# Kernel tuning notes

Measured on AMD Instinct MI355X. Metric: run time of the kernel, lower is better.

## Reference

```python
import jax, jax.numpy as jnp
import numpy as np
from jax import lax

FPLANE = 256
RATIO = 0.5
C_SHIFT = int(FPLANE * RATIO)  # 128
HALF = C_SHIFT // 2            # 64


def setup_inputs() -> dict:
    key = jax.random.key(0)
    k_x, k_wl, k_bl, k_wr, k_br = jax.random.split(key, 5)
    T, C, H, W = 64, FPLANE, 56, 56
    x = jax.random.normal(k_x, (T, C, H, W), dtype=jnp.float32)
    # Conv3d(HALF -> 1, kernel (3,3,3)); original inits to zero, we use small
    # random weights so the gated path is non-trivial for kernel testing.
    scale = 1.0 / np.sqrt(HALF * 27)
    w_l = jax.random.normal(k_wl, (1, HALF, 3, 3, 3), dtype=jnp.float32) * scale
    b_l = jax.random.normal(k_bl, (1,), dtype=jnp.float32) * 0.01
    w_r = jax.random.normal(k_wr, (1, HALF, 3, 3, 3), dtype=jnp.float32) * scale
    b_r = jax.random.normal(k_br, (1,), dtype=jnp.float32) * 0.01
    return {"x": x, "w_l": w_l, "b_l": b_l, "w_r": w_r, "b_r": b_r}


def _cyclic_pad_t(x):
    # x: (1, C, T, H, W) -> pad 1 frame cyclically along T
    return jnp.concatenate([x[:, :, -1:], x, x[:, :, :1]], axis=2)


def _conv3d(x, w, b):
    # temporal padding VALID (input is cyclically pre-padded), spatial SAME
    y = lax.conv_general_dilated(
        x, w, window_strides=(1, 1, 1),
        padding=[(0, 0), (1, 1), (1, 1)],
        dimension_numbers=("NCDHW", "OIDHW", "NCDHW"))
    return y + b[None, :, None, None, None]


def reference(x, w_l, b_l, w_r, b_r):
    # x: (T, C, H, W) -> (1, C, T, H, W)
    x5 = x.transpose(1, 0, 2, 3)[None]
    x_l = x5[:, :HALF]                 # (1, half, T, H, W)
    x_r = x5[:, HALF:C_SHIFT]
    x_keep = x5[:, C_SHIFT:]

    gate_l = jnp.tanh(_conv3d(_cyclic_pad_t(x_l), w_l, b_l))  # (1,1,T,H,W)
    gate_r = jnp.tanh(_conv3d(_cyclic_pad_t(x_r), w_r, b_r))

    y_l = gate_l * x_l
    y_r = gate_r * x_r
    y_l = jnp.roll(y_l, -1, axis=2) + (x_l - y_l)
    y_r = jnp.roll(y_r, 1, axis=2) + (x_r - y_r)

    y_all = jnp.concatenate([y_l, y_r, x_keep], axis=1)  # (1, C, T, H, W)
    return y_all[0].transpose(1, 0, 2, 3)                # (T, C, H, W)
```

## Files before the change

### kernel.cpp

```cpp
#include <hip/hip_runtime.h>
#include <math.h>

#define T_DIM 64
#define C_DIM 256
#define H_DIM 56
#define W_DIM 56
#define HW    (H_DIM * W_DIM)
#define HW4   (HW / 4)
#define CHW   (C_DIM * HW)
#define THW   (T_DIM * HW)

typedef float nt_float4 __attribute__((ext_vector_type(4)));

__device__ __forceinline__ float rfl(float v) {
    return __int_as_float(__builtin_amdgcn_readfirstlane(__float_as_int(v)));
}

template<int S>
__global__ __launch_bounds__(256) void gate_copy_kernel(
    const float* __restrict__ x,
    const float* __restrict__ w_l,
    const float* __restrict__ w_r,
    float* __restrict__ pbuf,
    float* __restrict__ out)
{
    constexpr int CPG   = 64 / S;
    constexpr int NGATE = 2 * S * 32;

    const int p = blockIdx.x;

    if (p >= NGATE) {
        const int qq     = p - NGATE;
        const int tchunk = qq / 392;
        const int bx2    = qq - tchunk * 392;
        const int tid    = 128 * HW4 + bx2 * 256 + (int)threadIdx.x;
        const int t0     = tchunk * 16;

        const nt_float4* xn4 = (const nt_float4*)x;
        nt_float4*       on4 = (nt_float4*)out;
        const size_t ts = C_DIM * HW4;

        #pragma unroll 4
        for (int i = 0; i < 16; ++i) {
            const size_t idx = (size_t)(t0 + i) * ts + tid;
            nt_float4 v = __builtin_nontemporal_load(&xn4[idx]);
            __builtin_nontemporal_store(v, &on4[idx]);
        }
        return;
    }

    const int xcd = p & 7;
    const int s   = p >> 3;
    const int sg  = xcd * (2 * S / 8) + (s >> 5);
    const int tq  = s & 31;
    const int side = sg / S;
    const int g    = sg & (S - 1);

    const int waveid = __builtin_amdgcn_readfirstlane((int)(threadIdx.x >> 6));
    const int hh = waveid & 1;
    const int t  = tq * 2 + (waveid >> 1);

    const int lane = threadIdx.x & 63;
    const int wg   = lane & 15;
    const int rg   = lane >> 4;
    const bool act = (wg < 14);
    const int w0   = act ? wg * 4 : 52;
    const int r0   = hh * 28 + rg * 7;
    const bool have_l = (wg > 0);
    const bool have_r = (wg < 13);

    const float* wtab = (side ? w_r : w_l) + g * CPG * 27;
    const int c0 = side * 64 + g * CPG;

    const int tm = (t + 63) & 63, tp = (t + 1) & 63;
    const float* tbase[3] = { x + (size_t)tm * CHW,
                              x + (size_t)t  * CHW,
                              x + (size_t)tp * CHW };

    float acc[7][4];
    #pragma unroll
    for (int j = 0; j < 7; ++j)
        #pragma unroll
        for (int k = 0; k < 4; ++k) acc[j][k] = 0.f;

    #pragma unroll 1
    for (int ci = 0; ci < CPG; ++ci) {
        float wgt[27];
        #pragma unroll
        for (int k = 0; k < 27; ++k) wgt[k] = rfl(wtab[ci * 27 + k]);

        #pragma unroll
        for (int dt = 0; dt < 3; ++dt) {
            const float* plane = tbase[dt] + (size_t)(c0 + ci) * HW;

            #pragma unroll
            for (int s9 = 0; s9 < 9; ++s9) {
                const int sr = r0 - 1 + s9;
                bool rv = true;
                int  srow = sr;
                if (s9 == 0)      { rv = (sr >= 0);     srow = rv ? sr : 0; }
                else if (s9 == 8) { rv = (sr < H_DIM);  srow = rv ? sr : (H_DIM - 1); }

                const float* row = plane + srow * W_DIM;
                float4 m  = *(const float4*)(row + w0);
                float  fl = __shfl_up(m.w, 1);
                float  fr = __shfl_down(m.x, 1);

                float f0 = have_l ? fl : 0.f;
                float f1 = m.x, f2 = m.y, f3 = m.z, f4v = m.w;
                float f5 = have_r ? fr : 0.f;
                if ((s9 == 0 || s9 == 8) && !rv) {
                    f0 = 0.f; f1 = 0.f; f2 = 0.f; f3 = 0.f; f4v = 0.f; f5 = 0.f;
                }
                float f[6] = { f0, f1, f2, f3, f4v, f5 };

                const int jlo = (s9 >= 2) ? s9 - 2 : 0;
                const int jhi = (s9 <= 6) ? s9 : 6;
                #pragma unroll
                for (int j = jlo; j <= jhi; ++j) {
                    const int dh = s9 - j;
                    const float w0t = wgt[dt * 9 + dh * 3 + 0];
                    const float w1t = wgt[dt * 9 + dh * 3 + 1];
                    const float w2t = wgt[dt * 9 + dh * 3 + 2];
                    #pragma unroll
                    for (int k = 0; k < 4; ++k)
                        acc[j][k] += w0t * f[k] + w1t * f[k + 1] + w2t * f[k + 2];
                }
            }
        }
    }

    if (act) {
        float* pp = pbuf + (size_t)sg * THW
                         + (size_t)t * HW + r0 * W_DIM + w0;
        #pragma unroll
        for (int j = 0; j < 7; ++j) {
            float4 v; v.x = acc[j][0]; v.y = acc[j][1]; v.z = acc[j][2]; v.w = acc[j][3];
            *(float4*)(pp + j * W_DIM) = v;
        }
    }
}

template<int S>
__global__ __launch_bounds__(256) void reduce_tanh_kernel(
    const float* __restrict__ pbuf,
    float* __restrict__ gbuf,
    const float* __restrict__ b_l,
    const float* __restrict__ b_r)
{
    const int i = blockIdx.x * 256 + threadIdx.x;
    const float4* p4 = (const float4*)pbuf;
    float4* g4 = (float4*)gbuf;

    float4 a = {0.f,0.f,0.f,0.f}, b = {0.f,0.f,0.f,0.f};
    #pragma unroll
    for (int g = 0; g < S; ++g) {
        float4 va = p4[(size_t)g       * (THW/4) + i];
        float4 vb = p4[(size_t)(S + g) * (THW/4) + i];
        a.x += va.x; a.y += va.y; a.z += va.z; a.w += va.w;
        b.x += vb.x; b.y += vb.y; b.z += vb.z; b.w += vb.w;
    }
    const float bl = b_l[0], br = b_r[0];
    float4 gl, gr;
    gl.x = tanhf(a.x + bl); gl.y = tanhf(a.y + bl);
    gl.z = tanhf(a.z + bl); gl.w = tanhf(a.w + bl);
    gr.x = tanhf(b.x + br); gr.y = tanhf(b.y + br);
    gr.z = tanhf(b.z + br); gr.w = tanhf(b.w + br);
    g4[i]           = gl;
    g4[(THW/4) + i] = gr;
}

__global__ __launch_bounds__(256) void combine_kernel(
    const float* __restrict__ x,
    const float* __restrict__ g,
    float* __restrict__ out)
{
    const int tid = blockIdx.x * 256 + threadIdx.x;
    const int t0  = blockIdx.y * 16;
    const int c   = tid / HW4;
    const int gb  = tid - c * HW4;

    const float4* x4 = (const float4*)x;
    nt_float4*    on4 = (nt_float4*)out;
    const size_t  ts = C_DIM * HW4;
    const size_t  base = tid;

    if (c < 64) {
        const float4* gl4 = (const float4*)g;
        float4 xv = x4[(size_t)t0 * ts + base];
        float4 g0 = gl4[t0 * HW4 + gb];
        #pragma unroll 4
        for (int i = 0; i < 16; ++i) {
            const int t  = t0 + i;
            const int tp = (t + 1) & 63;
            float4 xn = x4[(size_t)tp * ts + base];
            float4 g1 = gl4[tp * HW4 + gb];
            nt_float4 r;
            r.x = xv.x - g0.x * xv.x + g1.x * xn.x;
            r.y = xv.y - g0.y * xv.y + g1.y * xn.y;
            r.z = xv.z - g0.z * xv.z + g1.z * xn.z;
            r.w = xv.w - g0.w * xv.w + g1.w * xn.w;
            __builtin_nontemporal_store(r, &on4[(size_t)t * ts + base]);
            xv = xn; g0 = g1;
        }
    } else {
        const float4* gr4 = (const float4*)(g + THW);
        const int tmi = (t0 + 63) & 63;
        float4 xm = x4[(size_t)tmi * ts + base];
        float4 gm = gr4[tmi * HW4 + gb];
        #pragma unroll 4
        for (int i = 0; i < 16; ++i) {
            const int t = t0 + i;
            float4 xv = x4[(size_t)t * ts + base];
            float4 g0 = gr4[t * HW4 + gb];
            nt_float4 r;
            r.x = xv.x - g0.x * xv.x + gm.x * xm.x;
            r.y = xv.y - g0.y * xv.y + gm.y * xm.y;
            r.z = xv.z - g0.z * xv.z + gm.z * xm.z;
            r.w = xv.w - g0.w * xv.w + gm.w * xm.w;
            __builtin_nontemporal_store(r, &on4[(size_t)t * ts + base]);
            xm = xv; gm = g0;
        }
    }
}

template<int S>
static void launch_all(const float* x, const float* w_l, const float* b_l,
                       const float* w_r, const float* b_r,
                       float* out, float* ws, hipStream_t stream)
{
    float* pbuf = ws;
    float* gbuf = ws + (size_t)(2 * S) * THW;

    const int ngate = 2 * S * 32;
    const int ncopy = 392 * 4;
    gate_copy_kernel<S><<<ngate + ncopy, 256, 0, stream>>>(x, w_l, w_r, pbuf, out);
    reduce_tanh_kernel<S><<<THW / 4 / 256, 256, 0, stream>>>(pbuf, gbuf, b_l, b_r);
    combine_kernel<<<dim3(392, 4), 256, 0, stream>>>(x, gbuf, out);
}

extern "C" void kernel_launch(void* const* d_in, const int* in_sizes, int n_in,
                              void* d_out, int out_size, void* d_ws, size_t ws_size,
                              hipStream_t stream) {
    const float* x   = (const float*)d_in[0];
    const float* w_l = (const float*)d_in[1];
    const float* b_l = (const float*)d_in[2];
    const float* w_r = (const float*)d_in[3];
    const float* b_r = (const float*)d_in[4];
    float* out = (float*)d_out;
    float* ws  = (float*)d_ws;

    const size_t plane_bytes = (size_t)THW * 4;
    if (ws_size >= 34 * plane_bytes)
        launch_all<16>(x, w_l, b_l, w_r, b_r, out, ws, stream);
    else if (ws_size >= 18 * plane_bytes)
        launch_all<8>(x, w_l, b_l, w_r, b_r, out, ws, stream);
    else
        launch_all<4>(x, w_l, b_l, w_r, b_r, out, ws, stream);
}
```

Measured before the change: 110.2 us.

## Fuse channel-partial reduction and tanh into gate kernel via LDS

The gate conv kernel now assigns 16 input channels to each of four waves in a block and reduces the four partial sums through shared memory, then applies the bias and tanh directly. This replaces writing many per-group partial planes to the workspace and running a separate reduce/tanh kernel. It removes a large global-memory round trip and a kernel launch. The cost is fewer gate blocks, each with a longer serial channel loop, plus a block barrier.

```diff
diff --git a/kernel.cpp b/kernel.cpp
--- a/kernel.cpp
+++ b/kernel.cpp
@@ -16,17 +16,16 @@
     return __int_as_float(__builtin_amdgcn_readfirstlane(__float_as_int(v)));
 }
 
-template<int S>
 __global__ __launch_bounds__(256) void gate_copy_kernel(
     const float* __restrict__ x,
     const float* __restrict__ w_l,
+    const float* __restrict__ b_l,
     const float* __restrict__ w_r,
-    float* __restrict__ pbuf,
+    const float* __restrict__ b_r,
+    float* __restrict__ gbuf,
     float* __restrict__ out)
 {
-    constexpr int CPG   = 64 / S;
-    constexpr int NGATE = 2 * S * 32;
-
+    constexpr int NGATE = 256;
     const int p = blockIdx.x;
 
     if (p >= NGATE) {
@@ -49,17 +48,16 @@
         return;
     }
 
-    const int xcd = p & 7;
-    const int s   = p >> 3;
-    const int sg  = xcd * (2 * S / 8) + (s >> 5);
-    const int tq  = s & 31;
-    const int side = sg / S;
-    const int g    = sg & (S - 1);
+    __shared__ float4 red[4][7][64];
+
+    const int xcd  = p & 7;
+    const int r    = p >> 3;
+    const int tl   = r & 7;
+    const int side = (r >> 3) & 1;
+    const int hh   = (r >> 4) & 1;
+    const int t    = xcd * 8 + tl;
 
     const int waveid = __builtin_amdgcn_readfirstlane((int)(threadIdx.x >> 6));
-    const int hh = waveid & 1;
-    const int t  = tq * 2 + (waveid >> 1);
-
     const int lane = threadIdx.x & 63;
     const int wg   = lane & 15;
     const int rg   = lane >> 4;
@@ -69,8 +67,8 @@
     const bool have_l = (wg > 0);
     const bool have_r = (wg < 13);
 
-    const float* wtab = (side ? w_r : w_l) + g * CPG * 27;
-    const int c0 = side * 64 + g * CPG;
+    const float* wtab = (side ? w_r : w_l) + waveid * 16 * 27;
+    const int c0 = side * 64 + waveid * 16;
 
     const int tm = (t + 63) & 63, tp = (t + 1) & 63;
     const float* tbase[3] = { x + (size_t)tm * CHW,
@@ -84,7 +82,7 @@
         for (int k = 0; k < 4; ++k) acc[j][k] = 0.f;
 
     #pragma unroll 1
-    for (int ci = 0; ci < CPG; ++ci) {
+    for (int ci = 0; ci < 16; ++ci) {
         float wgt[27];
         #pragma unroll
         for (int k = 0; k < 27; ++k) wgt[k] = rfl(wtab[ci * 27 + k]);
@@ -130,44 +128,29 @@
         }
     }
 
-    if (act) {
-        float* pp = pbuf + (size_t)sg * THW
+    #pragma unroll
+    for (int j = 0; j < 7; ++j) {
+        float4 v; v.x = acc[j][0]; v.y = acc[j][1]; v.z = acc[j][2]; v.w = acc[j][3];
+        red[waveid][j][lane] = v;
+    }
+    __syncthreads();
+
+    if (waveid == 0 && act) {
+        const float bias = side ? b_r[0] : b_l[0];
+        float* pp = gbuf + (size_t)side * THW
                          + (size_t)t * HW + r0 * W_DIM + w0;
         #pragma unroll
         for (int j = 0; j < 7; ++j) {
-            float4 v; v.x = acc[j][0]; v.y = acc[j][1]; v.z = acc[j][2]; v.w = acc[j][3];
+            float4 a = red[0][j][lane], b2 = red[1][j][lane];
+            float4 c = red[2][j][lane], d  = red[3][j][lane];
+            float4 v;
+            v.x = tanhf((a.x + b2.x) + (c.x + d.x) + bias);
+            v.y = tanhf((a.y + b2.y) + (c.y + d.y) + bias);
+            v.z = tanhf((a.z + b2.z) + (c.z + d.z) + bias);
+            v.w = tanhf((a.w + b2.w) + (c.w + d.w) + bias);
             *(float4*)(pp + j * W_DIM) = v;
         }
     }
-}
-
-template<int S>
-__global__ __launch_bounds__(256) void reduce_tanh_kernel(
-    const float* __restrict__ pbuf,
-    float* __restrict__ gbuf,
-    const float* __restrict__ b_l,
-    const float* __restrict__ b_r)
-{
-    const int i = blockIdx.x * 256 + threadIdx.x;
-    const float4* p4 = (const float4*)pbuf;
-    float4* g4 = (float4*)gbuf;
-
-    float4 a = {0.f,0.f,0.f,0.f}, b = {0.f,0.f,0.f,0.f};
-    #pragma unroll
-    for (int g = 0; g < S; ++g) {
-        float4 va = p4[(size_t)g       * (THW/4) + i];
-        float4 vb = p4[(size_t)(S + g) * (THW/4) + i];
-        a.x += va.x; a.y += va.y; a.z += va.z; a.w += va.w;
-        b.x += vb.x; b.y += vb.y; b.z += vb.z; b.w += vb.w;
-    }
-    const float bl = b_l[0], br = b_r[0];
-    float4 gl, gr;
-    gl.x = tanhf(a.x + bl); gl.y = tanhf(a.y + bl);
-    gl.z = tanhf(a.z + bl); gl.w = tanhf(a.w + bl);
-    gr.x = tanhf(b.x + br); gr.y = tanhf(b.y + br);
-    gr.z = tanhf(b.z + br); gr.w = tanhf(b.w + br);
-    g4[i]           = gl;
-    g4[(THW/4) + i] = gr;
 }
 
 __global__ __launch_bounds__(256) void combine_kernel(
@@ -224,21 +207,6 @@
     }
 }
 
-template<int S>
-static void launch_all(const float* x, const float* w_l, const float* b_l,
-                       const float* w_r, const float* b_r,
-                       float* out, float* ws, hipStream_t stream)
-{
-    float* pbuf = ws;
-    float* gbuf = ws + (size_t)(2 * S) * THW;
-
-    const int ngate = 2 * S * 32;
-    const int ncopy = 392 * 4;
-    gate_copy_kernel<S><<<ngate + ncopy, 256, 0, stream>>>(x, w_l, w_r, pbuf, out);
-    reduce_tanh_kernel<S><<<THW / 4 / 256, 256, 0, stream>>>(pbuf, gbuf, b_l, b_r);
-    combine_kernel<<<dim3(392, 4), 256, 0, stream>>>(x, gbuf, out);
-}
-
 extern "C" void kernel_launch(void* const* d_in, const int* in_sizes, int n_in,
                               void* d_out, int out_size, void* d_ws, size_t ws_size,
                               hipStream_t stream) {
@@ -247,14 +215,12 @@
     const float* b_l = (const float*)d_in[2];
     const float* w_r = (const float*)d_in[3];
     const float* b_r = (const float*)d_in[4];
-    float* out = (float*)d_out;
-    float* ws  = (float*)d_ws;
-
-    const size_t plane_bytes = (size_t)THW * 4;
-    if (ws_size >= 34 * plane_bytes)
-        launch_all<16>(x, w_l, b_l, w_r, b_r, out, ws, stream);
-    else if (ws_size >= 18 * plane_bytes)
-        launch_all<8>(x, w_l, b_l, w_r, b_r, out, ws, stream);
-    else
-        launch_all<4>(x, w_l, b_l, w_r, b_r, out, ws, stream);
-}
+    float* out  = (float*)d_out;
+    float* gbuf = (float*)d_ws;
+
+    const int ngate = 256;
+    const int ncopy = 392 * 4;
+    gate_copy_kernel<<<ngate + ncopy, 256, 0, stream>>>(x, w_l, b_l, w_r, b_r,
+                                                        gbuf, out);
+    combine_kernel<<<dim3(392, 4), 256, 0, stream>>>(x, gbuf, out);
+}
```

Result: slower. 125.9 us (+14.2%).

## Fuse gate, reduce and combine into one cooperative kernel with grid syncs

Applied to the files above, without the earlier changes.

Replaces the three-kernel pipeline (gate+copy, reduce+tanh, combine) with a single cooperative kernel of 1024 blocks that uses grid-wide syncs between the phases. It also changes the gate decomposition to 4 channel groups per side, so there are fewer partial planes to reduce, and interleaves the copy and gate work across blocks. The aim is to remove launch gaps and shrink partial-sum traffic. The cost is two grid barriers and a less parallel combine phase. The fallback path is now fixed to S=16 if the cooperative launch fails or too little workspace is available.

```diff
diff --git a/kernel.cpp b/kernel.cpp
--- a/kernel.cpp
+++ b/kernel.cpp
@@ -1,5 +1,8 @@
 #include <hip/hip_runtime.h>
+#include <hip/hip_cooperative_groups.h>
 #include <math.h>
+
+namespace cg = cooperative_groups;
 
 #define T_DIM 64
 #define C_DIM 256
@@ -9,11 +12,230 @@
 #define HW4   (HW / 4)
 #define CHW   (C_DIM * HW)
 #define THW   (T_DIM * HW)
+#define PL4   (THW / 4)
+#define TS4   (C_DIM * HW4)
+#define NCOL  (128 * HW4)
+#define NCOPY4 (T_DIM * NCOL)
+#define GRID_F 1024
+#define GSZ   (GRID_F * 256)
 
 typedef float nt_float4 __attribute__((ext_vector_type(4)));
 
 __device__ __forceinline__ float rfl(float v) {
     return __int_as_float(__builtin_amdgcn_readfirstlane(__float_as_int(v)));
+}
+
+__global__ __launch_bounds__(256) void fused_all(
+    const float* __restrict__ x,
+    const float* __restrict__ w_l,
+    const float* __restrict__ b_l,
+    const float* __restrict__ w_r,
+    const float* __restrict__ b_r,
+    float* __restrict__ pbuf,
+    float* __restrict__ gbuf,
+    float* __restrict__ out)
+{
+    cg::grid_group grid = cg::this_grid();
+    __shared__ float4 red[4][7][64];
+
+    const int p    = blockIdx.x;
+    const int tid  = threadIdx.x;
+    const int gtid = p * 256 + tid;
+
+    const int rr   = p >> 3;
+    const int tl   = rr & 7;
+    const int side = (rr >> 3) & 1;
+    const int hh   = (rr >> 4) & 1;
+    const int gq   = (rr >> 5) & 3;
+    const int t    = (p & 7) * 8 + tl;
+
+    const int waveid = __builtin_amdgcn_readfirstlane(tid >> 6);
+    const int lane = tid & 63;
+    const int wg   = lane & 15;
+    const int rg   = lane >> 4;
+    const bool act = (wg < 14);
+    const int w0   = act ? wg * 4 : 52;
+    const int r0   = hh * 28 + rg * 7;
+    const bool have_l = (wg > 0);
+    const bool have_r = (wg < 13);
+
+    auto do_copy = [&]() {
+        const nt_float4* xn4 = (const nt_float4*)x;
+        nt_float4*       on4 = (nt_float4*)out;
+        for (int i = gtid; i < NCOPY4; i += GSZ) {
+            const int tt = i / NCOL;
+            const int rc = i - tt * NCOL;
+            const size_t idx = (size_t)tt * TS4 + NCOL + rc;
+            nt_float4 v = __builtin_nontemporal_load(&xn4[idx]);
+            __builtin_nontemporal_store(v, &on4[idx]);
+        }
+    };
+
+    auto do_gate = [&]() {
+        const int cw = gq * 16 + waveid * 4;
+        const float* wtab = (side ? w_r : w_l) + cw * 27;
+        const int c0 = side * 64 + cw;
+
+        const int tm = (t + 63) & 63, tp = (t + 1) & 63;
+        const float* tbase[3] = { x + (size_t)tm * CHW,
+                                  x + (size_t)t  * CHW,
+                                  x + (size_t)tp * CHW };
+
+        float acc[7][4];
+        #pragma unroll
+        for (int j = 0; j < 7; ++j)
+            #pragma unroll
+            for (int k = 0; k < 4; ++k) acc[j][k] = 0.f;
+
+        #pragma unroll 1
+        for (int ci = 0; ci < 4; ++ci) {
+            float wgt[27];
+            #pragma unroll
+            for (int k = 0; k < 27; ++k) wgt[k] = rfl(wtab[ci * 27 + k]);
+
+            #pragma unroll
+            for (int dt = 0; dt < 3; ++dt) {
+                const float* plane = tbase[dt] + (size_t)(c0 + ci) * HW;
+
+                #pragma unroll
+                for (int s9 = 0; s9 < 9; ++s9) {
+                    const int sr = r0 - 1 + s9;
+                    bool rv = true;
+                    int  srow = sr;
+                    if (s9 == 0)      { rv = (sr >= 0);     srow = rv ? sr : 0; }
+                    else if (s9 == 8) { rv = (sr < H_DIM);  srow = rv ? sr : (H_DIM - 1); }
+
+                    const float* row = plane + srow * W_DIM;
+                    float4 m  = *(const float4*)(row + w0);
+                    float  fl = __shfl_up(m.w, 1);
+                    float  fr = __shfl_down(m.x, 1);
+
+                    float f0 = have_l ? fl : 0.f;
+                    float f1 = m.x, f2 = m.y, f3 = m.z, f4v = m.w;
+                    float f5 = have_r ? fr : 0.f;
+                    if ((s9 == 0 || s9 == 8) && !rv) {
+                        f0 = 0.f; f1 = 0.f; f2 = 0.f; f3 = 0.f; f4v = 0.f; f5 = 0.f;
+                    }
+                    float f[6] = { f0, f1, f2, f3, f4v, f5 };
+
+                    const int jlo = (s9 >= 2) ? s9 - 2 : 0;
+                    const int jhi = (s9 <= 6) ? s9 : 6;
+                    #pragma unroll
+                    for (int j = jlo; j <= jhi; ++j) {
+                        const int dh = s9 - j;
+                        const float w0t = wgt[dt * 9 + dh * 3 + 0];
+                        const float w1t = wgt[dt * 9 + dh * 3 + 1];
+                        const float w2t = wgt[dt * 9 + dh * 3 + 2];
+                        #pragma unroll
+                        for (int k = 0; k < 4; ++k)
+                            acc[j][k] += w0t * f[k] + w1t * f[k + 1] + w2t * f[k + 2];
+                    }
+                }
+            }
+        }
+
+        #pragma unroll
+        for (int j = 0; j < 7; ++j) {
+            float4 v; v.x = acc[j][0]; v.y = acc[j][1];
+                      v.z = acc[j][2]; v.w = acc[j][3];
+            red[waveid][j][lane] = v;
+        }
+        __syncthreads();
+
+        if (waveid == 0 && act) {
+            const int sg = side * 4 + gq;
+            float* pp = pbuf + (size_t)sg * THW
+                             + (size_t)t * HW + r0 * W_DIM + w0;
+            #pragma unroll
+            for (int j = 0; j < 7; ++j) {
+                float4 a = red[0][j][lane], b2 = red[1][j][lane];
+                float4 c = red[2][j][lane], d  = red[3][j][lane];
+                float4 v;
+                v.x = (a.x + b2.x) + (c.x + d.x);
+                v.y = (a.y + b2.y) + (c.y + d.y);
+                v.z = (a.z + b2.z) + (c.z + d.z);
+                v.w = (a.w + b2.w) + (c.w + d.w);
+                *(float4*)(pp + j * W_DIM) = v;
+            }
+        }
+    };
+
+    if (p & 1) { do_copy(); do_gate(); }
+    else       { do_gate(); do_copy(); }
+
+    grid.sync();
+
+    if (gtid < PL4) {
+        const float4* p4 = (const float4*)pbuf;
+        float4* g4 = (float4*)gbuf;
+        float4 a = {0.f,0.f,0.f,0.f}, b = {0.f,0.f,0.f,0.f};
+        #pragma unroll
+        for (int g = 0; g < 4; ++g) {
+            float4 va = p4[(size_t)g       * PL4 + gtid];
+            float4 vb = p4[(size_t)(4 + g) * PL4 + gtid];
+            a.x += va.x; a.y += va.y; a.z += va.z; a.w += va.w;
+            b.x += vb.x; b.y += vb.y; b.z += vb.z; b.w += vb.w;
+        }
+        const float bl = b_l[0], br = b_r[0];
+        float4 gl, gr;
+        gl.x = tanhf(a.x + bl); gl.y = tanhf(a.y + bl);
+        gl.z = tanhf(a.z + bl); gl.w = tanhf(a.w + bl);
+        gr.x = tanhf(b.x + br); gr.y = tanhf(b.y + br);
+        gr.z = tanhf(b.z + br); gr.w = tanhf(b.w + br);
+        g4[gtid]       = gl;
+        g4[PL4 + gtid] = gr;
+    }
+
+    grid.sync();
+
+    if (gtid < 2 * NCOL) {
+        const int chunk = (gtid >= NCOL);
+        const int col   = gtid - chunk * NCOL;
+        const int c     = col / HW4;
+        const int gb    = col - c * HW4;
+        const int t0    = chunk * 32;
+
+        const float4* x4 = (const float4*)x;
+        nt_float4*    on4 = (nt_float4*)out;
+        const float4* g4 = (const float4*)gbuf;
+
+        if (c < 64) {
+            float4 xv = x4[(size_t)t0 * TS4 + col];
+            float4 g0 = g4[t0 * HW4 + gb];
+            #pragma unroll 4
+            for (int i = 0; i < 32; ++i) {
+                const int tt = t0 + i;
+                const int tp2 = (tt + 1) & 63;
+                float4 xn = x4[(size_t)tp2 * TS4 + col];
+                float4 g1 = g4[tp2 * HW4 + gb];
+                nt_float4 r;
+                r.x = xv.x - g0.x * xv.x + g1.x * xn.x;
+                r.y = xv.y - g0.y * xv.y + g1.y * xn.y;
+                r.z = xv.z - g0.z * xv.z + g1.z * xn.z;
+                r.w = xv.w - g0.w * xv.w + g1.w * xn.w;
+                __builtin_nontemporal_store(r, &on4[(size_t)tt * TS4 + col]);
+                xv = xn; g0 = g1;
+            }
+        } else {
+            const float4* gr4 = g4 + PL4;
+            const int tmi = (t0 + 63) & 63;
+            float4 xm = x4[(size_t)tmi * TS4 + col];
+            float4 gm = gr4[tmi * HW4 + gb];
+            #pragma unroll 4
+            for (int i = 0; i < 32; ++i) {
+                const int tt = t0 + i;
+                float4 xv = x4[(size_t)tt * TS4 + col];
+                float4 g0 = gr4[tt * HW4 + gb];
+                nt_float4 r;
+                r.x = xv.x - g0.x * xv.x + gm.x * xm.x;
+                r.y = xv.y - g0.y * xv.y + gm.y * xm.y;
+                r.z = xv.z - g0.z * xv.z + gm.z * xm.z;
+                r.w = xv.w - g0.w * xv.w + gm.w * xm.w;
+                __builtin_nontemporal_store(r, &on4[(size_t)tt * TS4 + col]);
+                xm = xv; gm = g0;
+            }
+        }
+    }
 }
 
 template<int S>
@@ -38,11 +260,10 @@
 
         const nt_float4* xn4 = (const nt_float4*)x;
         nt_float4*       on4 = (nt_float4*)out;
-        const size_t ts = C_DIM * HW4;
 
         #pragma unroll 4
         for (int i = 0; i < 16; ++i) {
-            const size_t idx = (size_t)(t0 + i) * ts + tid;
+            const size_t idx = (size_t)(t0 + i) * TS4 + tid;
             nt_float4 v = __builtin_nontemporal_load(&xn4[idx]);
             __builtin_nontemporal_store(v, &on4[idx]);
         }
@@ -155,8 +376,8 @@
     float4 a = {0.f,0.f,0.f,0.f}, b = {0.f,0.f,0.f,0.f};
     #pragma unroll
     for (int g = 0; g < S; ++g) {
-        float4 va = p4[(size_t)g       * (THW/4) + i];
-        float4 vb = p4[(size_t)(S + g) * (THW/4) + i];
+        float4 va = p4[(size_t)g       * PL4 + i];
+        float4 vb = p4[(size_t)(S + g) * PL4 + i];
         a.x += va.x; a.y += va.y; a.z += va.z; a.w += va.w;
         b.x += vb.x; b.y += vb.y; b.z += vb.z; b.w += vb.w;
     }
@@ -166,8 +387,8 @@
     gl.z = tanhf(a.z + bl); gl.w = tanhf(a.w + bl);
     gr.x = tanhf(b.x + br); gr.y = tanhf(b.y + br);
     gr.z = tanhf(b.z + br); gr.w = tanhf(b.w + br);
-    g4[i]           = gl;
-    g4[(THW/4) + i] = gr;
+    g4[i]       = gl;
+    g4[PL4 + i] = gr;
 }
 
 __global__ __launch_bounds__(256) void combine_kernel(
@@ -182,61 +403,45 @@
 
     const float4* x4 = (const float4*)x;
     nt_float4*    on4 = (nt_float4*)out;
-    const size_t  ts = C_DIM * HW4;
     const size_t  base = tid;
 
     if (c < 64) {
         const float4* gl4 = (const float4*)g;
-        float4 xv = x4[(size_t)t0 * ts + base];
+        float4 xv = x4[(size_t)t0 * TS4 + base];
         float4 g0 = gl4[t0 * HW4 + gb];
         #pragma unroll 4
         for (int i = 0; i < 16; ++i) {
             const int t  = t0 + i;
             const int tp = (t + 1) & 63;
-            float4 xn = x4[(size_t)tp * ts + base];
+            float4 xn = x4[(size_t)tp * TS4 + base];
             float4 g1 = gl4[tp * HW4 + gb];
             nt_float4 r;
             r.x = xv.x - g0.x * xv.x + g1.x * xn.x;
             r.y = xv.y - g0.y * xv.y + g1.y * xn.y;
             r.z = xv.z - g0.z * xv.z + g1.z * xn.z;
             r.w = xv.w - g0.w * xv.w + g1.w * xn.w;
-            __builtin_nontemporal_store(r, &on4[(size_t)t * ts + base]);
+            __builtin_nontemporal_store(r, &on4[(size_t)t * TS4 + base]);
             xv = xn; g0 = g1;
         }
     } else {
         const float4* gr4 = (const float4*)(g + THW);
         const int tmi = (t0 + 63) & 63;
-        float4 xm = x4[(size_t)tmi * ts + base];
+        float4 xm = x4[(size_t)tmi * TS4 + base];
         float4 gm = gr4[tmi * HW4 + gb];
         #pragma unroll 4
         for (int i = 0; i < 16; ++i) {
             const int t = t0 + i;
-            float4 xv = x4[(size_t)t * ts + base];
+            float4 xv = x4[(size_t)t * TS4 + base];
             float4 g0 = gr4[t * HW4 + gb];
             nt_float4 r;
             r.x = xv.x - g0.x * xv.x + gm.x * xm.x;
             r.y = xv.y - g0.y * xv.y + gm.y * xm.y;
             r.z = xv.z - g0.z * xv.z + gm.z * xm.z;
             r.w = xv.w - g0.w * xv.w + gm.w * xm.w;
-            __builtin_nontemporal_store(r, &on4[(size_t)t * ts + base]);
+            __builtin_nontemporal_store(r, &on4[(size_t)t * TS4 + base]);
             xm = xv; gm = g0;
         }
     }
-}
-
-template<int S>
-static void launch_all(const float* x, const float* w_l, const float* b_l,
-                       const float* w_r, const float* b_r,
-                       float* out, float* ws, hipStream_t stream)
-{
-    float* pbuf = ws;
-    float* gbuf = ws + (size_t)(2 * S) * THW;
-
-    const int ngate = 2 * S * 32;
-    const int ncopy = 392 * 4;
-    gate_copy_kernel<S><<<ngate + ncopy, 256, 0, stream>>>(x, w_l, w_r, pbuf, out);
-    reduce_tanh_kernel<S><<<THW / 4 / 256, 256, 0, stream>>>(pbuf, gbuf, b_l, b_r);
-    combine_kernel<<<dim3(392, 4), 256, 0, stream>>>(x, gbuf, out);
 }
 
 extern "C" void kernel_launch(void* const* d_in, const int* in_sizes, int n_in,
@@ -247,14 +452,34 @@
     const float* b_l = (const float*)d_in[2];
     const float* w_r = (const float*)d_in[3];
     const float* b_r = (const float*)d_in[4];
-    float* out = (float*)d_out;
-    float* ws  = (float*)d_ws;
-
+    float* out  = (float*)d_out;
+    float* ws   = (float*)d_ws;
+
+    int nb = 0;
+    hipError_t oe = hipOccupancyMaxActiveBlocksPerMultiprocessor(
+        &nb, reinterpret_cast<const void*>(&fused_all), 256, 0);
     const size_t plane_bytes = (size_t)THW * 4;
-    if (ws_size >= 34 * plane_bytes)
-        launch_all<16>(x, w_l, b_l, w_r, b_r, out, ws, stream);
-    else if (ws_size >= 18 * plane_bytes)
-        launch_all<8>(x, w_l, b_l, w_r, b_r, out, ws, stream);
-    else
-        launch_all<4>(x, w_l, b_l, w_r, b_r, out, ws, stream);
-}
+    bool try_coop = (oe == hipSuccess) && (nb >= 4) &&
+                    (ws_size >= 10 * plane_bytes);
+
+    if (try_coop) {
+        float* pbuf = ws;
+        float* gbuf = ws + (size_t)8 * THW;
+        void* args[8] = { (void*)&x, (void*)&w_l, (void*)&b_l,
+                          (void*)&w_r, (void*)&b_r,
+                          (void*)&pbuf, (void*)&gbuf, (void*)&out };
+        hipError_t le = hipLaunchCooperativeKernel(
+            reinterpret_cast<const void*>(&fused_all),
+            dim3(GRID_F), dim3(256), args, 0, stream);
+        if (le == hipSuccess) return;
+    }
+
+    constexpr int S = 16;
+    float* pbuf = ws;
+    float* gbuf = ws + (size_t)(2 * S) * THW;
+    const int ngate = 2 * S * 32;
+    const int ncopy = 392 * 4;
+    gate_copy_kernel<S><<<ngate + ncopy, 256, 0, stream>>>(x, w_l, w_r, pbuf, out);
+    reduce_tanh_kernel<S><<<PL4 / 256, 256, 0, stream>>>(pbuf, gbuf, b_l, b_r);
+    combine_kernel<<<dim3(392, 4), 256, 0, stream>>>(x, gbuf, out);
+}
```

New measurement: 110.0 us. Within noise of the previous version (-0.2%).

## Interleave passthrough channel copy into gate conv blocks to overlap memory traffic

Applied to the files above, without the earlier changes.

Moves part of the copy of the untouched channels (128..255) into the gate-conv blocks: each conv block copies a 4096-float4 slice, spread across its channel loop iterations, and only the remaining slices get dedicated copy blocks. The aim is to overlap the bandwidth-bound copy with the compute-heavy convolution and to cut the number of copy-only blocks. The cost is extra register and memory pressure inside the conv loop, and the copy indexing now uses a flat-index divide.

```diff
diff --git a/kernel.cpp b/kernel.cpp
--- a/kernel.cpp
+++ b/kernel.cpp
@@ -9,11 +9,24 @@
 #define HW4   (HW / 4)
 #define CHW   (C_DIM * HW)
 #define THW   (T_DIM * HW)
+#define PL4   (THW / 4)
+#define TS4   (C_DIM * HW4)
+#define NCOL  (128 * HW4)
+#define NCOPY4 (T_DIM * NCOL)
 
 typedef float nt_float4 __attribute__((ext_vector_type(4)));
 
 __device__ __forceinline__ float rfl(float v) {
     return __int_as_float(__builtin_amdgcn_readfirstlane(__float_as_int(v)));
+}
+
+__device__ __forceinline__ void copy_f4(const nt_float4* xn4, nt_float4* on4,
+                                        int i ) {
+    const int tt = i / NCOL;
+    const int rc = i - tt * NCOL;
+    const size_t idx = (size_t)tt * TS4 + NCOL + rc;
+    nt_float4 v = __builtin_nontemporal_load(&xn4[idx]);
+    __builtin_nontemporal_store(v, &on4[idx]);
 }
 
 template<int S>
@@ -25,27 +38,19 @@
     float* __restrict__ out)
 {
     constexpr int CPG   = 64 / S;
+    constexpr int KP    = 16 / CPG;
     constexpr int NGATE = 2 * S * 32;
 
-    const int p = blockIdx.x;
+    const int p   = blockIdx.x;
+    const int tid = threadIdx.x;
+    const nt_float4* xn4 = (const nt_float4*)x;
+    nt_float4*       on4 = (nt_float4*)out;
 
     if (p >= NGATE) {
-        const int qq     = p - NGATE;
-        const int tchunk = qq / 392;
-        const int bx2    = qq - tchunk * 392;
-        const int tid    = 128 * HW4 + bx2 * 256 + (int)threadIdx.x;
-        const int t0     = tchunk * 16;
-
-        const nt_float4* xn4 = (const nt_float4*)x;
-        nt_float4*       on4 = (nt_float4*)out;
-        const size_t ts = C_DIM * HW4;
-
+        const int base = NGATE * 4096 + (p - NGATE) * 4096;
         #pragma unroll 4
-        for (int i = 0; i < 16; ++i) {
-            const size_t idx = (size_t)(t0 + i) * ts + tid;
-            nt_float4 v = __builtin_nontemporal_load(&xn4[idx]);
-            __builtin_nontemporal_store(v, &on4[idx]);
-        }
+        for (int k = 0; k < 16; ++k)
+            copy_f4(xn4, on4, base + k * 256 + tid);
         return;
     }
 
@@ -56,11 +61,13 @@
     const int side = sg / S;
     const int g    = sg & (S - 1);
 
-    const int waveid = __builtin_amdgcn_readfirstlane((int)(threadIdx.x >> 6));
+    const int cbase = p * 4096 + tid;
+
+    const int waveid = __builtin_amdgcn_readfirstlane(tid >> 6);
     const int hh = waveid & 1;
     const int t  = tq * 2 + (waveid >> 1);
 
-    const int lane = threadIdx.x & 63;
+    const int lane = tid & 63;
     const int wg   = lane & 15;
     const int rg   = lane >> 4;
     const bool act = (wg < 14);
@@ -85,6 +92,10 @@
 
     #pragma unroll 1
     for (int ci = 0; ci < CPG; ++ci) {
+        #pragma unroll
+        for (int k = 0; k < KP; ++k)
+            copy_f4(xn4, on4, cbase + (ci * KP + k) * 256);
+
         float wgt[27];
         #pragma unroll
         for (int k = 0; k < 27; ++k) wgt[k] = rfl(wtab[ci * 27 + k]);
@@ -155,8 +166,8 @@
     float4 a = {0.f,0.f,0.f,0.f}, b = {0.f,0.f,0.f,0.f};
     #pragma unroll
     for (int g = 0; g < S; ++g) {
-        float4 va = p4[(size_t)g       * (THW/4) + i];
-        float4 vb = p4[(size_t)(S + g) * (THW/4) + i];
+        float4 va = p4[(size_t)g       * PL4 + i];
+        float4 vb = p4[(size_t)(S + g) * PL4 + i];
         a.x += va.x; a.y += va.y; a.z += va.z; a.w += va.w;
         b.x += vb.x; b.y += vb.y; b.z += vb.z; b.w += vb.w;
     }
@@ -166,8 +177,8 @@
     gl.z = tanhf(a.z + bl); gl.w = tanhf(a.w + bl);
     gr.x = tanhf(b.x + br); gr.y = tanhf(b.y + br);
     gr.z = tanhf(b.z + br); gr.w = tanhf(b.w + br);
-    g4[i]           = gl;
-    g4[(THW/4) + i] = gr;
+    g4[i]       = gl;
+    g4[PL4 + i] = gr;
 }
 
 __global__ __launch_bounds__(256) void combine_kernel(
@@ -182,43 +193,42 @@
 
     const float4* x4 = (const float4*)x;
     nt_float4*    on4 = (nt_float4*)out;
-    const size_t  ts = C_DIM * HW4;
     const size_t  base = tid;
 
     if (c < 64) {
         const float4* gl4 = (const float4*)g;
-        float4 xv = x4[(size_t)t0 * ts + base];
+        float4 xv = x4[(size_t)t0 * TS4 + base];
         float4 g0 = gl4[t0 * HW4 + gb];
         #pragma unroll 4
         for (int i = 0; i < 16; ++i) {
             const int t  = t0 + i;
             const int tp = (t + 1) & 63;
-            float4 xn = x4[(size_t)tp * ts + base];
+            float4 xn = x4[(size_t)tp * TS4 + base];
             float4 g1 = gl4[tp * HW4 + gb];
             nt_float4 r;
             r.x = xv.x - g0.x * xv.x + g1.x * xn.x;
             r.y = xv.y - g0.y * xv.y + g1.y * xn.y;
             r.z = xv.z - g0.z * xv.z + g1.z * xn.z;
             r.w = xv.w - g0.w * xv.w + g1.w * xn.w;
-            __builtin_nontemporal_store(r, &on4[(size_t)t * ts + base]);
+            __builtin_nontemporal_store(r, &on4[(size_t)t * TS4 + base]);
             xv = xn; g0 = g1;
         }
     } else {
         const float4* gr4 = (const float4*)(g + THW);
         const int tmi = (t0 + 63) & 63;
-        float4 xm = x4[(size_t)tmi * ts + base];
+        float4 xm = x4[(size_t)tmi * TS4 + base];
         float4 gm = gr4[tmi * HW4 + gb];
         #pragma unroll 4
         for (int i = 0; i < 16; ++i) {
             const int t = t0 + i;
-            float4 xv = x4[(size_t)t * ts + base];
+            float4 xv = x4[(size_t)t * TS4 + base];
             float4 g0 = gr4[t * HW4 + gb];
             nt_float4 r;
             r.x = xv.x - g0.x * xv.x + gm.x * xm.x;
             r.y = xv.y - g0.y * xv.y + gm.y * xm.y;
             r.z = xv.z - g0.z * xv.z + gm.z * xm.z;
             r.w = xv.w - g0.w * xv.w + gm.w * xm.w;
-            __builtin_nontemporal_store(r, &on4[(size_t)t * ts + base]);
+            __builtin_nontemporal_store(r, &on4[(size_t)t * TS4 + base]);
             xm = xv; gm = g0;
         }
     }
@@ -233,9 +243,12 @@
     float* gbuf = ws + (size_t)(2 * S) * THW;
 
     const int ngate = 2 * S * 32;
-    const int ncopy = 392 * 4;
+    const int gate_copy = ngate * 4096;
+    const int rem = NCOPY4 - gate_copy;
+    const int ncopy = rem / 4096;
+
     gate_copy_kernel<S><<<ngate + ncopy, 256, 0, stream>>>(x, w_l, w_r, pbuf, out);
-    reduce_tanh_kernel<S><<<THW / 4 / 256, 256, 0, stream>>>(pbuf, gbuf, b_l, b_r);
+    reduce_tanh_kernel<S><<<PL4 / 256, 256, 0, stream>>>(pbuf, gbuf, b_l, b_r);
     combine_kernel<<<dim3(392, 4), 256, 0, stream>>>(x, gbuf, out);
 }
 
```

Measured after the change: 107.4 us, median of 2. 1.03x faster.
